# Performance work log

Measured on AMD Instinct MI355X. Metric: run time of the kernel, lower is better.

Reference implementation:

```python
import jax, jax.numpy as jnp
import numpy as np
import math

IN_DIM, OUT_DIM, NUM_BASIS = 256, 128, 6
MAX_IN_SEQ, MAX_OUT_SEQ = 512, 256
REDUCTION = 2
LN_EPS = 1e-5


def setup_inputs() -> dict:
    key = jax.random.key(0)
    ks = jax.random.split(key, 8)
    u = lambda k, shape, a: jax.random.uniform(k, shape, jnp.float32, -a, a)
    x = jax.random.normal(ks[0], (16, MAX_IN_SEQ, IN_DIM), jnp.float32)
    M = u(ks[1], (OUT_DIM, IN_DIM), 0.5)
    P = u(ks[2], (OUT_DIM, OUT_DIM, NUM_BASIS), 0.1)
    Linker = u(ks[3], (MAX_IN_SEQ, MAX_OUT_SEQ), 0.1)
    ln_gamma = jnp.ones((OUT_DIM,), jnp.float32)
    ln_beta = jnp.zeros((OUT_DIM,), jnp.float32)
    res_W = u(ks[4], (OUT_DIM, IN_DIM), 0.1)
    res_linker = u(ks[5], (MAX_IN_SEQ, MAX_OUT_SEQ), 0.1)
    # periods[i,j,g] = i*(out_dim*num_basis) + j*num_basis + g + 2 (non-trainable buffer)
    periods = (jnp.arange(OUT_DIM * OUT_DIM * NUM_BASIS, dtype=jnp.float32)
               .reshape(OUT_DIM, OUT_DIM, NUM_BASIS) + 2.0)
    return {"x": x, "M": M, "P": P, "Linker": Linker, "ln_gamma": ln_gamma,
            "ln_beta": ln_beta, "res_W": res_W, "res_linker": res_linker,
            "periods": periods, "actual_seq_len": 512}


def _layer_norm(z, gamma, beta):
    mu = jnp.mean(z, axis=-1, keepdims=True)
    var = jnp.var(z, axis=-1, keepdims=True)
    return (z - mu) * jax.lax.rsqrt(var + LN_EPS) * gamma + beta


def reference(x, M, P, Linker, ln_gamma, ln_beta, res_W, res_linker, periods, actual_seq_len):
    b, seq_len, _ = x.shape
    # Z = LN(x @ M^T)
    Z = _layer_norm(jnp.matmul(x, M.T), ln_gamma, ln_beta)  # (b, s, out)
    # position-dependent trig basis: phi[s,i,j,g] = cos(2*pi*s / periods[i,j,g])
    k = jnp.arange(seq_len, dtype=jnp.float32)[:, None, None, None]
    phi = jnp.cos(2.0 * math.pi * k / periods[None])          # (s, out, out, nb)
    # fold basis into per-position mixing matrix, then contract (matches sum over dims 3,4)
    W = jnp.einsum('ijg,sijg->sij', P, phi)                   # (s, out, out)
    T = jnp.einsum('bsj,sij->bsi', Z, W)                      # (b, s, out)
    # adaptive linker: reduce sequence length
    L = actual_seq_len
    Lo = max(1, L // REDUCTION)
    U = jnp.einsum('bsi,so->boi', T[:, :L], Linker[:L, :Lo])  # (b, out_seq, out)
    # 'separate' residual
    rfeat = jnp.matmul(x[:, :L], res_W.T)                     # (b, s, out)
    residual = jnp.einsum('bsi,so->boi', rfeat, res_linker[:L, :Lo])
    return U + residual
```

## Files before the change

### kernel.cpp

```cpp
#include <hip/hip_runtime.h>
#include <hip/hip_bf16.h>

#define LN_EPS 1e-5f

typedef __attribute__((ext_vector_type(8))) short short8;
typedef __attribute__((ext_vector_type(4))) float floatx4;

__device__ __forceinline__ float bf2f(unsigned int u16) {
    union { unsigned int i; float f; } v; v.i = (u16 & 0xffffu) << 16; return v.f;
}
__device__ __forceinline__ unsigned short f2bf(float f) {
    __hip_bfloat16 h = __float2bfloat16(f);
    union { __hip_bfloat16 h; unsigned short u; } v; v.h = h; return v.u;
}
__device__ __forceinline__ unsigned int pack2(float a, float b) {
    return (unsigned int)f2bf(a) | ((unsigned int)f2bf(b) << 16);
}
__device__ __forceinline__ short8 pack8(float4 a, float4 b) {
    union { short8 s; uint4 u; } v;
    v.u.x = pack2(a.x, a.y); v.u.y = pack2(a.z, a.w);
    v.u.z = pack2(b.x, b.y); v.u.w = pack2(b.z, b.w);
    return v.s;
}

union SMem {
    struct { float buf[32 * 258]; float red1[256]; float red2[256]; float mus[32]; float rsg[32]; } p1;
    unsigned short lcat[32 * 260];
};

__global__ __launch_bounds__(256) void s1_produce(const float* __restrict__ x,
                                                  const float* __restrict__ M,
                                                  const float* __restrict__ resW,
                                                  const float* __restrict__ gamma,
                                                  const float* __restrict__ beta,
                                                  const float* __restrict__ P,
                                                  const float* __restrict__ periods,
                                                  const float* __restrict__ Linker,
                                                  const float* __restrict__ resL,
                                                  unsigned short* __restrict__ Z,
                                                  unsigned short* __restrict__ TRt,
                                                  unsigned short* __restrict__ W,
                                                  unsigned short* __restrict__ LcatT) {
    __shared__ SMem sm;
    int blk = blockIdx.x, t = threadIdx.x;
    int w = t >> 6, l = t & 63;
    int lane15 = l & 15, quad = l >> 4;

    if (blk < 512) {
        int et = blk & 31, sc = blk >> 5;
        int e0 = et * 512 + t * 2;
        const float* pp = P + (size_t)e0 * 6;
        float4 pa = *(const float4*)(pp);
        float4 pb = *(const float4*)(pp + 4);
        float4 pc = *(const float4*)(pp + 8);
        float pf[12] = { pa.x, pa.y, pa.z, pa.w, pb.x, pb.y, pb.z, pb.w, pc.x, pc.y, pc.z, pc.w };
        const float* qp = periods + (size_t)e0 * 6;
        float4 qa = *(const float4*)(qp);
        float4 qb = *(const float4*)(qp + 4);
        float4 qc = *(const float4*)(qp + 8);
        float iv[12] = { __builtin_amdgcn_rcpf(qa.x), __builtin_amdgcn_rcpf(qa.y),
                         __builtin_amdgcn_rcpf(qa.z), __builtin_amdgcn_rcpf(qa.w),
                         __builtin_amdgcn_rcpf(qb.x), __builtin_amdgcn_rcpf(qb.y),
                         __builtin_amdgcn_rcpf(qb.z), __builtin_amdgcn_rcpf(qb.w),
                         __builtin_amdgcn_rcpf(qc.x), __builtin_amdgcn_rcpf(qc.y),
                         __builtin_amdgcn_rcpf(qc.z), __builtin_amdgcn_rcpf(qc.w) };
        float s0f = (float)(sc * 32);
        float tc[12], cm1[12], cc[12];
        #pragma unroll
        for (int g = 0; g < 12; ++g) {
            tc[g]  = 2.0f * __builtin_amdgcn_cosf(iv[g]);
            cm1[g] = __builtin_amdgcn_cosf(__builtin_amdgcn_fractf(s0f * iv[g]));
            cc[g]  = __builtin_amdgcn_cosf(__builtin_amdgcn_fractf((s0f + 1.0f) * iv[g]));
        }
        #pragma unroll 4
        for (int ss = 0; ss < 32; ++ss) {
            float a0 = 0.f, a1 = 0.f;
            #pragma unroll
            for (int g = 0; g < 6; ++g)  a0 += pf[g] * cm1[g];
            #pragma unroll
            for (int g = 6; g < 12; ++g) a1 += pf[g] * cm1[g];
            int s = sc * 32 + ss;
            *(unsigned int*)(W + (size_t)s * 16384 + e0) = pack2(a0, a1);
            #pragma unroll
            for (int g = 0; g < 12; ++g) {
                float cn = fmaf(tc[g], cc[g], -cm1[g]);
                cm1[g] = cc[g]; cc[g] = cn;
            }
        }
    } else if (blk < 768) {
        int r0 = (blk - 512) * 32;
        const float* wbase = (w < 2) ? M : resW;
        int wco = (w < 2) ? (w * 64) : (w * 64 - 128);
        floatx4 acc[2][4] = {};
        for (int kk = 0; kk < 256; kk += 32) {
            int k0 = kk + quad * 8;
            const float* xr0 = x + (size_t)(r0 + lane15) * 256 + k0;
            const float* xr1 = x + (size_t)(r0 + 16 + lane15) * 256 + k0;
            short8 a0 = pack8(*(const float4*)xr0, *(const float4*)(xr0 + 4));
            short8 a1 = pack8(*(const float4*)xr1, *(const float4*)(xr1 + 4));
            #pragma unroll
            for (int nt = 0; nt < 4; ++nt) {
                const float* br = wbase + (size_t)(wco + nt * 16 + lane15) * 256 + k0;
                short8 b = pack8(*(const float4*)br, *(const float4*)(br + 4));
                acc[0][nt] = __builtin_amdgcn_mfma_f32_16x16x32_bf16(a0, b, acc[0][nt], 0, 0, 0);
                acc[1][nt] = __builtin_amdgcn_mfma_f32_16x16x32_bf16(a1, b, acc[1][nt], 0, 0, 0);
            }
        }
        #pragma unroll
        for (int mt = 0; mt < 2; ++mt)
            #pragma unroll
            for (int nt = 0; nt < 4; ++nt)
                #pragma unroll
                for (int r = 0; r < 4; ++r) {
                    int ro = mt * 16 + quad * 4 + r;
                    int co = w * 64 + nt * 16 + lane15;
                    sm.p1.buf[ro * 258 + co] = acc[mt][nt][r];
                }
        __syncthreads();
        {
            int r = t >> 3, seg = t & 7;
            float s1 = 0.f, s2 = 0.f;
            #pragma unroll
            for (int e = 0; e < 16; ++e) { float v = sm.p1.buf[r * 258 + seg * 16 + e]; s1 += v; s2 += v * v; }
            sm.p1.red1[r * 8 + seg] = s1; sm.p1.red2[r * 8 + seg] = s2;
        }
        __syncthreads();
        if (t < 32) {
            float s1 = 0.f, s2 = 0.f;
            #pragma unroll
            for (int e = 0; e < 8; ++e) { s1 += sm.p1.red1[t * 8 + e]; s2 += sm.p1.red2[t * 8 + e]; }
            float mu = s1 * (1.0f / 128.0f);
            float var = s2 * (1.0f / 128.0f) - mu * mu;
            sm.p1.mus[t] = mu; sm.p1.rsg[t] = rsqrtf(var + LN_EPS);
        }
        __syncthreads();
        int b = r0 >> 9, s0 = r0 & 511;
        {
            int r = t >> 3, c0 = (t & 7) * 16;
            int grow = r0 + r;
            float mu = sm.p1.mus[r], rs = sm.p1.rsg[r];
            float zv[16];
            #pragma unroll
            for (int e = 0; e < 16; ++e) {
                int j = c0 + e;
                zv[e] = (sm.p1.buf[r * 258 + j] - mu) * rs * gamma[j] + beta[j];
            }
            uint4 oz0, oz1;
            oz0.x = pack2(zv[0], zv[1]);  oz0.y = pack2(zv[2], zv[3]);
            oz0.z = pack2(zv[4], zv[5]);  oz0.w = pack2(zv[6], zv[7]);
            oz1.x = pack2(zv[8], zv[9]);  oz1.y = pack2(zv[10], zv[11]);
            oz1.z = pack2(zv[12], zv[13]); oz1.w = pack2(zv[14], zv[15]);
            *(uint4*)(Z + (size_t)grow * 128 + c0) = oz0;
            *(uint4*)(Z + (size_t)grow * 128 + c0 + 8) = oz1;
        }
        {
            int j = t >> 1, sh = (t & 1) * 16;
            unsigned int ow[8];
            #pragma unroll
            for (int p = 0; p < 8; ++p) {
                float v0 = sm.p1.buf[(sh + 2 * p) * 258 + 128 + j];
                float v1 = sm.p1.buf[(sh + 2 * p + 1) * 258 + 128 + j];
                ow[p] = pack2(v0, v1);
            }
            unsigned short* dst = TRt + ((size_t)b * 128 + j) * 1024 + 512 + s0 + sh;
            uint4 u0; u0.x = ow[0]; u0.y = ow[1]; u0.z = ow[2]; u0.w = ow[3];
            uint4 u1; u1.x = ow[4]; u1.y = ow[5]; u1.z = ow[6]; u1.w = ow[7];
            *(uint4*)(dst) = u0;
            *(uint4*)(dst + 8) = u1;
        }
    } else {
        int kb = blk - 768;
        int k0 = kb * 32;
        const float* src = (kb < 16) ? (Linker + (size_t)k0 * 256)
                                     : (resL + (size_t)(k0 - 512) * 256);
        #pragma unroll
        for (int q = 0; q < 8; ++q) {
            int lin = t + 256 * q;
            int row = lin >> 6, col4 = (lin & 63) * 4;
            float4 v = *(const float4*)(src + row * 256 + col4);
            *(unsigned int*)(sm.lcat + row * 260 + col4)     = pack2(v.x, v.y);
            *(unsigned int*)(sm.lcat + row * 260 + col4 + 2) = pack2(v.z, v.w);
        }
        __syncthreads();
        int o = t;
        unsigned int outw[16];
        #pragma unroll
        for (int kp = 0; kp < 16; ++kp) {
            unsigned int lo = sm.lcat[(2 * kp) * 260 + o];
            unsigned int hi = sm.lcat[(2 * kp + 1) * 260 + o];
            outw[kp] = lo | (hi << 16);
        }
        unsigned short* dst = LcatT + (size_t)o * 1024 + k0;
        #pragma unroll
        for (int qq = 0; qq < 4; ++qq) {
            uint4 u; u.x = outw[qq*4]; u.y = outw[qq*4+1]; u.z = outw[qq*4+2]; u.w = outw[qq*4+3];
            *(uint4*)(dst + qq * 8) = u;
        }
    }
}

__global__ __launch_bounds__(256) void k2b_t(const unsigned short* __restrict__ W,
                                             const unsigned short* __restrict__ Z,
                                             unsigned short* __restrict__ TRt) {
    __shared__ unsigned short tbuf[16 * 64 * 4];
    int t = threadIdx.x, w = t >> 6, l = t & 63;
    int lane15 = l & 15, quad = l >> 4;
    int st = blockIdx.x >> 1, ih = blockIdx.x & 1;
    int s0 = st * 4;
    int i0 = ih * 64 + w * 16;
    #pragma unroll
    for (int ss = 0; ss < 4; ++ss) {
        int s = s0 + ss;
        floatx4 acc = {};
        #pragma unroll
        for (int kk = 0; kk < 4; ++kk) {
            int k0 = kk * 32 + quad * 8;
            short8 a  = *(const short8*)(Z + ((size_t)lane15 * 512 + s) * 128 + k0);
            short8 bf = *(const short8*)(W + (size_t)s * 16384 + (i0 + lane15) * 128 + k0);
            acc = __builtin_amdgcn_mfma_f32_16x16x32_bf16(a, bf, acc, 0, 0, 0);
        }
        int il = w * 16 + lane15;
        #pragma unroll
        for (int r = 0; r < 4; ++r) {
            int brow = quad * 4 + r;
            tbuf[(brow * 64 + il) * 4 + ss] = f2bf(acc[r]);
        }
    }
    __syncthreads();
    int ihb = ih * 64;
    #pragma unroll
    for (int q = 0; q < 4; ++q) {
        int p = t + 256 * q;
        int b = p >> 6, il = p & 63;
        uint2 v = *(const uint2*)(tbuf + p * 4);
        *(uint2*)(TRt + ((size_t)b * 128 + ihb + il) * 1024 + s0) = v;
    }
}

__global__ __launch_bounds__(256) void k3_out(const unsigned short* __restrict__ LcatT,
                                              const unsigned short* __restrict__ TRt,
                                              float* __restrict__ out) {
    __shared__ float red[4 * 32 * 64];
    int t = threadIdx.x, w = t >> 6, l = t & 63;
    int lane15 = l & 15, quad = l >> 4;
    int b = blockIdx.x, o0 = blockIdx.y * 32, i0 = blockIdx.z * 64;
    const unsigned short* trb = TRt + (size_t)b * 128 * 1024;
    floatx4 acc[2][4] = {};
    #pragma unroll 2
    for (int kk = 0; kk < 8; ++kk) {
        int k0 = w * 256 + kk * 32 + quad * 8;
        short8 afr0 = *(const short8*)(LcatT + (size_t)(o0 + lane15) * 1024 + k0);
        short8 afr1 = *(const short8*)(LcatT + (size_t)(o0 + 16 + lane15) * 1024 + k0);
        #pragma unroll
        for (int nt = 0; nt < 4; ++nt) {
            short8 bfr = *(const short8*)(trb + (size_t)(i0 + nt * 16 + lane15) * 1024 + k0);
            acc[0][nt] = __builtin_amdgcn_mfma_f32_16x16x32_bf16(afr0, bfr, acc[0][nt], 0, 0, 0);
            acc[1][nt] = __builtin_amdgcn_mfma_f32_16x16x32_bf16(afr1, bfr, acc[1][nt], 0, 0, 0);
        }
    }
    #pragma unroll
    for (int mt = 0; mt < 2; ++mt)
        #pragma unroll
        for (int nt = 0; nt < 4; ++nt)
            #pragma unroll
            for (int r = 0; r < 4; ++r) {
                int ro = mt * 16 + quad * 4 + r;
                int co = nt * 16 + lane15;
                red[(w * 32 + ro) * 64 + co] = acc[mt][nt][r];
            }
    __syncthreads();
    {
        int ro = t >> 3, c0 = (t & 7) * 8;
        float vs[8];
        #pragma unroll
        for (int e = 0; e < 8; ++e) {
            float sum = 0.f;
            #pragma unroll
            for (int ww = 0; ww < 4; ++ww) sum += red[(ww * 32 + ro) * 64 + c0 + e];
            vs[e] = sum;
        }
        float4 o1 = { vs[0], vs[1], vs[2], vs[3] };
        float4 o2 = { vs[4], vs[5], vs[6], vs[7] };
        size_t ob = ((size_t)b * 256 + o0 + ro) * 128 + i0 + c0;
        *(float4*)(out + ob) = o1;
        *(float4*)(out + ob + 4) = o2;
    }
}

extern "C" void kernel_launch(void* const* d_in, const int* in_sizes, int n_in,
                              void* d_out, int out_size, void* d_ws, size_t ws_size,
                              hipStream_t stream) {
    const float* x      = (const float*)d_in[0];
    const float* M      = (const float*)d_in[1];
    const float* P      = (const float*)d_in[2];
    const float* Linker = (const float*)d_in[3];
    const float* gamma  = (const float*)d_in[4];
    const float* beta   = (const float*)d_in[5];
    const float* resW   = (const float*)d_in[6];
    const float* resL   = (const float*)d_in[7];
    const float* periods= (const float*)d_in[8];
    (void)in_sizes; (void)n_in; (void)out_size; (void)ws_size;

    float* ws = (float*)d_ws;
    unsigned short* LcatT = (unsigned short*)(ws);
    unsigned short* Z     = (unsigned short*)(ws + 131072);
    unsigned short* TRt   = (unsigned short*)(ws + 655360);
    unsigned short* W     = (unsigned short*)(ws + 1703936);

    s1_produce<<<800, 256, 0, stream>>>(x, M, resW, gamma, beta, P, periods,
                                        Linker, resL, Z, TRt, W, LcatT);
    k2b_t<<<256, 256, 0, stream>>>(W, Z, TRt);
    k3_out<<<dim3(16, 8, 2), 256, 0, stream>>>(LcatT, TRt, (float*)d_out);
}
```

Before: 114.7 us.

## Store intermediates in k-chunked 8-element blocked layout for coalesced MFMA loads

Changes the global layouts of W, Z, TRt and LcatT so each group of 8 consecutive k-values for consecutive rows sits contiguously (k/8-major, then row, then 8 elements). Producers write in this blocked order and the MFMA consumers in k2b_t and k3_out read short8 fragments whose addresses are contiguous across lanes. The goal is to replace strided 1024- or 128-element row loads with coalesced 16-byte-per-lane accesses. In exchange, some producer stores become more scattered, for example the Z and TRt writes, and the index arithmetic is more involved.

```diff
diff --git a/kernel.cpp b/kernel.cpp
--- a/kernel.cpp
+++ b/kernel.cpp
@@ -3,12 +3,10 @@
 
 #define LN_EPS 1e-5f
 
+
 typedef __attribute__((ext_vector_type(8))) short short8;
 typedef __attribute__((ext_vector_type(4))) float floatx4;
 
-__device__ __forceinline__ float bf2f(unsigned int u16) {
-    union { unsigned int i; float f; } v; v.i = (u16 & 0xffffu) << 16; return v.f;
-}
 __device__ __forceinline__ unsigned short f2bf(float f) {
     __hip_bfloat16 h = __float2bfloat16(f);
     union { __hip_bfloat16 h; unsigned short u; } v; v.h = h; return v.u;
@@ -48,7 +46,9 @@
 
     if (blk < 512) {
         int et = blk & 31, sc = blk >> 5;
-        int e0 = et * 512 + t * 2;
+        int n0 = et * 512 + t * 2;
+        int jj = n0 & 7, ii = (n0 >> 3) & 127, qd = (n0 >> 10) & 3, kq = n0 >> 12;
+        int e0 = ii * 128 + kq * 32 + qd * 8 + jj;
         const float* pp = P + (size_t)e0 * 6;
         float4 pa = *(const float4*)(pp);
         float4 pb = *(const float4*)(pp + 4);
@@ -80,7 +80,7 @@
             #pragma unroll
             for (int g = 6; g < 12; ++g) a1 += pf[g] * cm1[g];
             int s = sc * 32 + ss;
-            *(unsigned int*)(W + (size_t)s * 16384 + e0) = pack2(a0, a1);
+            *(unsigned int*)(W + (size_t)s * 16384 + n0) = pack2(a0, a1);
             #pragma unroll
             for (int g = 0; g < 12; ++g) {
                 float cn = fmaf(tc[g], cc[g], -cm1[g]);
@@ -137,7 +137,7 @@
         int b = r0 >> 9, s0 = r0 & 511;
         {
             int r = t >> 3, c0 = (t & 7) * 16;
-            int grow = r0 + r;
+            int s_t = s0 + r;
             float mu = sm.p1.mus[r], rs = sm.p1.rsg[r];
             float zv[16];
             #pragma unroll
@@ -150,8 +150,9 @@
             oz0.z = pack2(zv[4], zv[5]);  oz0.w = pack2(zv[6], zv[7]);
             oz1.x = pack2(zv[8], zv[9]);  oz1.y = pack2(zv[10], zv[11]);
             oz1.z = pack2(zv[12], zv[13]); oz1.w = pack2(zv[14], zv[15]);
-            *(uint4*)(Z + (size_t)grow * 128 + c0) = oz0;
-            *(uint4*)(Z + (size_t)grow * 128 + c0 + 8) = oz1;
+            unsigned short* zdst = Z + (size_t)s_t * 2048 + (((c0 >> 3) * 16 + b) << 3);
+            *(uint4*)(zdst) = oz0;
+            *(uint4*)(zdst + 128) = oz1;
         }
         {
             int j = t >> 1, sh = (t & 1) * 16;
@@ -162,11 +163,12 @@
                 float v1 = sm.p1.buf[(sh + 2 * p + 1) * 258 + 128 + j];
                 ow[p] = pack2(v0, v1);
             }
-            unsigned short* dst = TRt + ((size_t)b * 128 + j) * 1024 + 512 + s0 + sh;
+            int kqA = 64 + ((s0 + sh) >> 3);
+            unsigned short* dst = TRt + (size_t)b * 131072 + ((size_t)(kqA * 128 + j) << 3);
             uint4 u0; u0.x = ow[0]; u0.y = ow[1]; u0.z = ow[2]; u0.w = ow[3];
             uint4 u1; u1.x = ow[4]; u1.y = ow[5]; u1.z = ow[6]; u1.w = ow[7];
             *(uint4*)(dst) = u0;
-            *(uint4*)(dst + 8) = u1;
+            *(uint4*)(dst + 1024) = u1;
         }
     } else {
         int kb = blk - 768;
@@ -190,11 +192,10 @@
             unsigned int hi = sm.lcat[(2 * kp + 1) * 260 + o];
             outw[kp] = lo | (hi << 16);
         }
-        unsigned short* dst = LcatT + (size_t)o * 1024 + k0;
         #pragma unroll
         for (int qq = 0; qq < 4; ++qq) {
             uint4 u; u.x = outw[qq*4]; u.y = outw[qq*4+1]; u.z = outw[qq*4+2]; u.w = outw[qq*4+3];
-            *(uint4*)(dst + qq * 8) = u;
+            *(uint4*)(LcatT + (((size_t)(kb * 4 + qq) * 256 + o) << 3)) = u;
         }
     }
 }
@@ -215,8 +216,8 @@
         #pragma unroll
         for (int kk = 0; kk < 4; ++kk) {
             int k0 = kk * 32 + quad * 8;
-            short8 a  = *(const short8*)(Z + ((size_t)lane15 * 512 + s) * 128 + k0);
-            short8 bf = *(const short8*)(W + (size_t)s * 16384 + (i0 + lane15) * 128 + k0);
+            short8 a  = *(const short8*)(Z + (size_t)s * 2048 + (((k0 >> 3) * 16 + lane15) << 3));
+            short8 bf = *(const short8*)(W + (size_t)s * 16384 + (((k0 >> 3) * 128 + i0 + lane15) << 3));
             acc = __builtin_amdgcn_mfma_f32_16x16x32_bf16(a, bf, acc, 0, 0, 0);
         }
         int il = w * 16 + lane15;
@@ -233,7 +234,7 @@
         int p = t + 256 * q;
         int b = p >> 6, il = p & 63;
         uint2 v = *(const uint2*)(tbuf + p * 4);
-        *(uint2*)(TRt + ((size_t)b * 128 + ihb + il) * 1024 + s0) = v;
+        *(uint2*)(TRt + (size_t)b * 131072 + (((s0 >> 3) * 128 + ihb + il) << 3) + (s0 & 7)) = v;
     }
 }
 
@@ -244,16 +245,17 @@
     int t = threadIdx.x, w = t >> 6, l = t & 63;
     int lane15 = l & 15, quad = l >> 4;
     int b = blockIdx.x, o0 = blockIdx.y * 32, i0 = blockIdx.z * 64;
-    const unsigned short* trb = TRt + (size_t)b * 128 * 1024;
+    const unsigned short* trb = TRt + (size_t)b * 131072;
     floatx4 acc[2][4] = {};
     #pragma unroll 2
     for (int kk = 0; kk < 8; ++kk) {
         int k0 = w * 256 + kk * 32 + quad * 8;
-        short8 afr0 = *(const short8*)(LcatT + (size_t)(o0 + lane15) * 1024 + k0);
-        short8 afr1 = *(const short8*)(LcatT + (size_t)(o0 + 16 + lane15) * 1024 + k0);
+        int kq = k0 >> 3;
+        short8 afr0 = *(const short8*)(LcatT + (((size_t)kq * 256 + o0 + lane15) << 3));
+        short8 afr1 = *(const short8*)(LcatT + (((size_t)kq * 256 + o0 + 16 + lane15) << 3));
         #pragma unroll
         for (int nt = 0; nt < 4; ++nt) {
-            short8 bfr = *(const short8*)(trb + (size_t)(i0 + nt * 16 + lane15) * 1024 + k0);
+            short8 bfr = *(const short8*)(trb + (((size_t)kq * 128 + i0 + nt * 16 + lane15) << 3));
             acc[0][nt] = __builtin_amdgcn_mfma_f32_16x16x32_bf16(afr0, bfr, acc[0][nt], 0, 0, 0);
             acc[1][nt] = __builtin_amdgcn_mfma_f32_16x16x32_bf16(afr1, bfr, acc[1][nt], 0, 0, 0);
         }
```

Measured after the change: 112.3 us. 2.1% less time.
